# Kernel optimization log

Hardware: AMD Instinct MI355X
Metric: run time of the kernel (lower is better)

The kernel has to match this reference:

```python
import jax, jax.numpy as jnp
import numpy as np

SEQ_LEN = 96
D_MODEL = 512
BATCH = 512
FREQ = SEQ_LEN // 2 + 1  # 49
EPS = 1e-5


def setup_inputs() -> dict:
    key = jax.random.key(0)
    ks = jax.random.split(key, 9)
    s = 1.0 / np.sqrt(D_MODEL)
    return {
        "x": jax.random.normal(ks[0], (BATCH, SEQ_LEN, D_MODEL), jnp.float32),
        "freq_weights": jnp.ones((FREQ,), jnp.float32),
        "Wl": jax.random.normal(ks[1], (D_MODEL, D_MODEL), jnp.float32) * s,
        "bl": jax.random.normal(ks[2], (D_MODEL,), jnp.float32) * s,
        "Wh": jax.random.normal(ks[3], (D_MODEL, D_MODEL), jnp.float32) * s,
        "bh": jax.random.normal(ks[4], (D_MODEL,), jnp.float32) * s,
        "Wg": jax.random.normal(ks[5], (2 * D_MODEL, D_MODEL), jnp.float32) * s,
        "bg": jax.random.normal(ks[6], (D_MODEL,), jnp.float32) * s,
        "gamma": jnp.ones((D_MODEL,), jnp.float32),
        "beta": jnp.zeros((D_MODEL,), jnp.float32),
    }


def reference(x, freq_weights, Wl, bl, Wh, bh, Wg, bg, gamma, beta):
    # Batched rfft over seq axis for all channels at once: [B, F, D] complex
    xf = jnp.fft.rfft(x, axis=1)
    xw = xf * freq_weights[None, :, None]
    cutoff = FREQ // 3  # 16 (static)
    idx = jnp.arange(FREQ)[None, :, None]
    x_low_f = jnp.where(idx < cutoff, xw, 0)
    x_high_f = jnp.where(idx >= cutoff, xw, 0)
    x_low = jnp.fft.irfft(x_low_f, n=SEQ_LEN, axis=1)   # [B, S, D]
    x_high = jnp.fft.irfft(x_high_f, n=SEQ_LEN, axis=1)
    x_low = jnp.einsum("bsd,de->bse", x_low, Wl) + bl
    x_high = jnp.einsum("bsd,de->bse", x_high, Wh) + bh
    gate_in = jnp.concatenate([x_low, x_high], axis=-1)  # [B, S, 2D]
    gate = jax.nn.sigmoid(jnp.einsum("bsd,de->bse", gate_in, Wg) + bg)
    out = gate * x_low + (1.0 - gate) * x_high
    y = x + out  # dropout is identity in eval mode
    mu = jnp.mean(y, axis=-1, keepdims=True)
    var = jnp.var(y, axis=-1, keepdims=True)
    return (y - mu) / jnp.sqrt(var + EPS) * gamma + beta
```

## Files before the change

### kernel.cpp

```cpp
#include <hip/hip_runtime.h>

typedef unsigned short u16;
typedef unsigned int u32;

#define SEQ 96
#define DM 512
#define NBATCH 512
#define NFREQ 49
#define CUT 16
#define MROWS (NBATCH * SEQ)

typedef __attribute__((ext_vector_type(8))) short bf16x8;
typedef __attribute__((ext_vector_type(4))) float f32x4;

__device__ __forceinline__ u16 f2bf(float f) {
  u32 u = __float_as_uint(f);
  u32 r = (u + 0x7fffu + ((u >> 16) & 1u)) >> 16;
  return (u16)r;
}
__device__ __forceinline__ float bf2f(u16 u) {
  return __uint_as_float(((u32)u) << 16);
}

__device__ __forceinline__ void g2l16(const void* g, void* l) {
  __builtin_amdgcn_global_load_lds(
      (const __attribute__((address_space(1))) void*)g,
      (__attribute__((address_space(3))) void*)l, 16, 0, 0);
}

__global__ void build_filters_k(const float* __restrict__ w,
                                u16* __restrict__ FlB, u16* __restrict__ FhB) {
  int idx = blockIdx.x * 256 + threadIdx.x;
  if (idx >= SEQ * SEQ) return;
  int s = idx / SEQ, t = idx % SEQ;
  int d = s - t;
  const float scale = 1.0f / (float)SEQ;
  const float w0 = 6.283185307179586f / (float)SEQ;
  float cl = 0.f, ch = 0.f;
  for (int k = 0; k < NFREQ; k++) {
    int m = (k * d) % SEQ;
    if (m < 0) m += SEQ;
    float c = (k == 0 || k == SEQ / 2) ? 1.0f : 2.0f;
    float v = c * w[k] * cosf(w0 * (float)m) * scale;
    if (k < CUT) cl += v; else ch += v;
  }
  FlB[idx] = f2bf(cl);
  FhB[idx] = f2bf(ch);
}

__global__ void __launch_bounds__(256) transpose_w_k(
    const float* __restrict__ W, u16* __restrict__ Wt, int K, int N) {
  __shared__ float t[32][33];
  int k0 = blockIdx.x * 32, n0 = blockIdx.y * 32;
  int tx = threadIdx.x & 31, ty = threadIdx.x >> 5;
  #pragma unroll
  for (int r = 0; r < 32; r += 8)
    t[ty + r][tx] = W[(size_t)(k0 + ty + r) * N + n0 + tx];
  __syncthreads();
  #pragma unroll
  for (int r = 0; r < 32; r += 8)
    Wt[(size_t)(n0 + ty + r) * K + k0 + tx] = f2bf(t[tx][ty + r]);
}

__global__ void __launch_bounds__(256) xb_k(const float* __restrict__ x,
                                            u16* __restrict__ xb) {
  size_t t = ((size_t)blockIdx.x * 256 + threadIdx.x) * 8;
  float4 f0 = *(const float4*)(x + t);
  float4 f1 = *(const float4*)(x + t + 4);
  uint4 o;
  o.x = (u32)f2bf(f0.x) | ((u32)f2bf(f0.y) << 16);
  o.y = (u32)f2bf(f0.z) | ((u32)f2bf(f0.w) << 16);
  o.z = (u32)f2bf(f1.x) | ((u32)f2bf(f1.y) << 16);
  o.w = (u32)f2bf(f1.z) | ((u32)f2bf(f1.w) << 16);
  *(uint4*)(xb + t) = o;
}

__global__ void __launch_bounds__(256) proj_dual_k(
    const u16* __restrict__ xb, const u16* __restrict__ Wt,
    u16* __restrict__ uT, u16* __restrict__ vT) {
  __shared__ __align__(16) u16 As[128 * 64];
  __shared__ __align__(16) u16 Bs[128 * 64];
  const int m0 = blockIdx.x * 128;
  const int n0 = blockIdx.y * 128;
  const int tid = threadIdx.x;
  const int lane = tid & 63;
  const int w = tid >> 6;
  const int wm = w & 1, wn = w >> 1;
  const int l15 = lane & 15;
  const int lq = lane >> 4;

  f32x4 acc[4][4] = {};

  for (int kt = 0; kt < 512; kt += 64) {
    #pragma unroll
    for (int r = 0; r < 4; r++) {
      int c = r * 256 + tid;
      int row = c >> 3;
      int off = (c & 7) << 3;
      u32 lo = (u32)((r * 256 + w * 64) << 4);
      g2l16(xb + (size_t)(m0 + row) * 512 + kt + off, (char*)As + lo);
      g2l16(Wt + (size_t)(n0 + row) * 512 + kt + off, (char*)Bs + lo);
    }
    __syncthreads();
    #pragma unroll
    for (int kk = 0; kk < 64; kk += 32) {
      bf16x8 af[4], bf[4];
      #pragma unroll
      for (int i = 0; i < 4; i++)
        af[i] = *(const bf16x8*)&As[(wm * 64 + i * 16 + l15) * 64 + kk + lq * 8];
      #pragma unroll
      for (int j = 0; j < 4; j++)
        bf[j] = *(const bf16x8*)&Bs[(wn * 64 + j * 16 + l15) * 64 + kk + lq * 8];
      #pragma unroll
      for (int i = 0; i < 4; i++)
        #pragma unroll
        for (int j = 0; j < 4; j++)
          acc[i][j] = __builtin_amdgcn_mfma_f32_16x16x32_bf16(af[i], bf[j], acc[i][j], 0, 0, 0);
    }
    __syncthreads();
  }

  #pragma unroll
  for (int j = 0; j < 4; j++) {
    int nv = n0 + wn * 64 + j * 16 + l15;
    u16* dst = (nv < 512) ? uT : vT;
    int e = nv & 511;
    #pragma unroll
    for (int i = 0; i < 4; i++) {
      int mbase = m0 + wm * 64 + i * 16 + lq * 4;
      int b = mbase / 96, s = mbase % 96;
      ushort4 st;
      st.x = f2bf(acc[i][j][0]);
      st.y = f2bf(acc[i][j][1]);
      st.z = f2bf(acc[i][j][2]);
      st.w = f2bf(acc[i][j][3]);
      *(ushort4*)&dst[((size_t)b * 512 + e) * SEQ + s] = st;
    }
  }
}

__global__ void __launch_bounds__(256) filter2_k(
    const u16* __restrict__ uT, const u16* __restrict__ vT,
    const u16* __restrict__ FlB, const u16* __restrict__ FhB,
    const float* __restrict__ bl, const float* __restrict__ bh,
    u16* __restrict__ yl, u16* __restrict__ yh) {
  __shared__ __align__(16) u16 lds[2 * SEQ * SEQ + 2 * 64 * SEQ];
  u16* Fls = lds;
  u16* Bu = lds + 2 * SEQ * SEQ;
  u16* Bv = Bu + 64 * SEQ;
  const int tid = threadIdx.x;
  const int lane = tid & 63, w = tid >> 6;
  const int b = blockIdx.x, d0 = blockIdx.y * 64;

  #pragma unroll
  for (int it = 0; it < 9; it++) {
    int c = it * 256 + tid;
    const u16* src = (c < 1152) ? (FlB + c * 8) : (FhB + (c - 1152) * 8);
    g2l16(src, (char*)Fls + ((it * 256 + w * 64) << 4));
  }
  const u16* bu = uT + ((size_t)b * 512 + d0) * SEQ;
  const u16* bv = vT + ((size_t)b * 512 + d0) * SEQ;
  #pragma unroll
  for (int it = 0; it < 3; it++) {
    int c = it * 256 + tid;
    int row = c / 12, off = (c % 12) * 8;
    u32 lo = (u32)((it * 256 + w * 64) << 4);
    g2l16(bu + (size_t)row * SEQ + off, (char*)Bu + lo);
    g2l16(bv + (size_t)row * SEQ + off, (char*)Bv + lo);
  }
  __syncthreads();

  const int wf = w >> 1, wd = w & 1;
  const int l15 = lane & 15, lq = lane >> 4;
  const u16* F = wf ? (Fls + SEQ * SEQ) : Fls;
  const u16* Bsrc = wf ? Bv : Bu;
  f32x4 acc[6][2] = {};
  #pragma unroll
  for (int ks = 0; ks < 3; ks++) {
    int kt = ks * 32;
    bf16x8 bf[2];
    #pragma unroll
    for (int j = 0; j < 2; j++)
      bf[j] = *(const bf16x8*)&Bsrc[(wd * 32 + j * 16 + l15) * SEQ + kt + lq * 8];
    #pragma unroll
    for (int i = 0; i < 6; i++) {
      bf16x8 af = *(const bf16x8*)&F[(i * 16 + l15) * SEQ + kt + lq * 8];
      #pragma unroll
      for (int j = 0; j < 2; j++)
        acc[i][j] = __builtin_amdgcn_mfma_f32_16x16x32_bf16(af, bf[j], acc[i][j], 0, 0, 0);
    }
  }
  const float* bias = wf ? bh : bl;
  u16* dst = wf ? yh : yl;
  #pragma unroll
  for (int j = 0; j < 2; j++) {
    int d = d0 + wd * 32 + j * 16 + l15;
    float bv2 = bias[d];
    #pragma unroll
    for (int i = 0; i < 6; i++)
      #pragma unroll
      for (int r = 0; r < 4; r++) {
        int s = i * 16 + lq * 4 + r;
        dst[((size_t)b * SEQ + s) * DM + d] = f2bf(acc[i][j][r] + bv2);
      }
  }
}

__global__ void __launch_bounds__(256) gemm_gate_mfma_k(
    const u16* __restrict__ yl, const u16* __restrict__ yh,
    const u16* __restrict__ Wgt, const float* __restrict__ bg,
    u16* __restrict__ g) {
  __shared__ __align__(16) u16 As[128 * 64];
  __shared__ __align__(16) u16 Bs[128 * 64];
  const int m0 = blockIdx.x * 128;
  const int n0 = blockIdx.y * 128;
  const int tid = threadIdx.x;
  const int lane = tid & 63;
  const int w = tid >> 6;
  const int wm = w & 1, wn = w >> 1;
  const int l15 = lane & 15;
  const int lq = lane >> 4;

  f32x4 acc[4][4] = {};

  for (int kt = 0; kt < 1024; kt += 64) {
    const u16* Ak = (kt < 512) ? yl : yh;
    int ka = kt & 511;
    #pragma unroll
    for (int r = 0; r < 4; r++) {
      int c = r * 256 + tid;
      int row = c >> 3;
      int off = (c & 7) << 3;
      u32 lo = (u32)((r * 256 + w * 64) << 4);
      g2l16(Ak + (size_t)(m0 + row) * 512 + ka + off, (char*)As + lo);
      g2l16(Wgt + (size_t)(n0 + row) * 1024 + kt + off, (char*)Bs + lo);
    }
    __syncthreads();
    #pragma unroll
    for (int kk = 0; kk < 64; kk += 32) {
      bf16x8 af[4], bf[4];
      #pragma unroll
      for (int i = 0; i < 4; i++)
        af[i] = *(const bf16x8*)&As[(wm * 64 + i * 16 + l15) * 64 + kk + lq * 8];
      #pragma unroll
      for (int j = 0; j < 4; j++)
        bf[j] = *(const bf16x8*)&Bs[(wn * 64 + j * 16 + l15) * 64 + kk + lq * 8];
      #pragma unroll
      for (int i = 0; i < 4; i++)
        #pragma unroll
        for (int j = 0; j < 4; j++)
          acc[i][j] = __builtin_amdgcn_mfma_f32_16x16x32_bf16(af[i], bf[j], acc[i][j], 0, 0, 0);
    }
    __syncthreads();
  }

  #pragma unroll
  for (int j = 0; j < 4; j++) {
    int n = n0 + wn * 64 + j * 16 + l15;
    float bv = bg[n];
    #pragma unroll
    for (int i = 0; i < 4; i++) {
      int mrow = m0 + wm * 64 + i * 16 + lq * 4;
      #pragma unroll
      for (int r = 0; r < 4; r++) {
        float z = acc[i][j][r] + bv;
        g[(size_t)(mrow + r) * 512 + n] = f2bf(1.0f / (1.0f + __expf(-z)));
      }
    }
  }
}

__global__ void __launch_bounds__(256) final_ln_k(
    const float* __restrict__ x, const u16* __restrict__ yl,
    const u16* __restrict__ yh, const u16* __restrict__ g,
    const float* __restrict__ gamma, const float* __restrict__ beta,
    float* __restrict__ out) {
  __shared__ float red[8];
  int r = blockIdx.x;
  size_t base = (size_t)r * 512;
  float vv[2];
  float sum = 0.f, sumsq = 0.f;
  #pragma unroll
  for (int j = 0; j < 2; j++) {
    int e = threadIdx.x + j * 256;
    float lv = bf2f(yl[base + e]);
    float hv = bf2f(yh[base + e]);
    float gv = bf2f(g[base + e]);
    float v = x[base + e] + gv * lv + (1.f - gv) * hv;
    vv[j] = v;
    sum += v;
    sumsq += v * v;
  }
  #pragma unroll
  for (int off = 32; off; off >>= 1) {
    sum += __shfl_down(sum, off);
    sumsq += __shfl_down(sumsq, off);
  }
  int wid = threadIdx.x >> 6;
  if ((threadIdx.x & 63) == 0) {
    red[wid] = sum;
    red[4 + wid] = sumsq;
  }
  __syncthreads();
  sum = red[0] + red[1] + red[2] + red[3];
  sumsq = red[4] + red[5] + red[6] + red[7];
  float mu = sum * (1.f / 512.f);
  float var = sumsq * (1.f / 512.f) - mu * mu;
  float inv = rsqrtf(var + 1e-5f);
  #pragma unroll
  for (int j = 0; j < 2; j++) {
    int e = threadIdx.x + j * 256;
    out[base + e] = (vv[j] - mu) * inv * gamma[e] + beta[e];
  }
}

extern "C" void kernel_launch(void* const* d_in, const int* in_sizes, int n_in,
                              void* d_out, int out_size, void* d_ws, size_t ws_size,
                              hipStream_t stream) {
  const float* x     = (const float*)d_in[0];
  const float* fw    = (const float*)d_in[1];
  const float* Wl    = (const float*)d_in[2];
  const float* bl    = (const float*)d_in[3];
  const float* Wh    = (const float*)d_in[4];
  const float* bh    = (const float*)d_in[5];
  const float* Wg    = (const float*)d_in[6];
  const float* bg    = (const float*)d_in[7];
  const float* gamma = (const float*)d_in[8];
  const float* beta  = (const float*)d_in[9];
  float* out = (float*)d_out;

  char* ws = (char*)d_ws;
  u16* FlB = (u16*)ws;
  u16* FhB = FlB + SEQ * SEQ;
  u16* Wt  = (u16*)(ws + 64 * 1024);
  u16* Wgt = Wt + 1024 * 512;
  size_t tsz = (size_t)MROWS * 512;
  u16* xb = (u16*)(ws + 4 * 1024 * 1024);
  u16* uT = xb + tsz;
  u16* vT = uT + tsz;
  u16* yh = vT + tsz;
  u16* yl = xb;
  u16* gb = uT;

  build_filters_k<<<dim3(36), dim3(256), 0, stream>>>(fw, FlB, FhB);
  transpose_w_k<<<dim3(16, 16), dim3(256), 0, stream>>>(Wl, Wt, 512, 512);
  transpose_w_k<<<dim3(16, 16), dim3(256), 0, stream>>>(Wh, Wt + 512 * 512, 512, 512);
  transpose_w_k<<<dim3(32, 16), dim3(256), 0, stream>>>(Wg, Wgt, 1024, 512);
  xb_k<<<dim3(MROWS * 512 / 2048), dim3(256), 0, stream>>>(x, xb);
  proj_dual_k<<<dim3(MROWS / 128, 8), dim3(256), 0, stream>>>(xb, Wt, uT, vT);
  filter2_k<<<dim3(NBATCH, DM / 64), dim3(256), 0, stream>>>(
      uT, vT, FlB, FhB, bl, bh, yl, yh);
  gemm_gate_mfma_k<<<dim3(MROWS / 128, 4), dim3(256), 0, stream>>>(yl, yh, Wgt, bg, gb);
  final_ln_k<<<dim3(MROWS), dim3(256), 0, stream>>>(x, yl, yh, gb, gamma, beta, out);
}
```

Baseline: 494.3 us.

## Fold gate GEMM into projection via precomputed Wl·Wg, Wh·Wg and fused tail

Uses linearity to precompute Wl@Wg_top and Wh@Wg_bot plus a combined gate bias, so the gate pre-activation becomes the filtered projections of x through these product matrices. A single wide GEMM now converts x to bf16 on the fly and produces four projections (u, v, p1, p2). One tail kernel per batch applies the low/high filters with MFMA, then computes the gate, the mix and the residual into the output. LayerNorm runs in place afterward. This drops the separate bf16 conversion, the 1024-K gate GEMM and the bf16 intermediates, at the cost of a wider projection GEMM (N=2048) and more bf16 rounding through the product weights.

```diff
diff --git a/kernel.cpp b/kernel.cpp
--- a/kernel.cpp
+++ b/kernel.cpp
@@ -17,9 +17,6 @@
   u32 u = __float_as_uint(f);
   u32 r = (u + 0x7fffu + ((u >> 16) & 1u)) >> 16;
   return (u16)r;
-}
-__device__ __forceinline__ float bf2f(u16 u) {
-  return __uint_as_float(((u32)u) << 16);
 }
 
 __device__ __forceinline__ void g2l16(const void* g, void* l) {
@@ -48,6 +45,60 @@
   FhB[idx] = f2bf(ch);
 }
 
+__global__ void __launch_bounds__(256) smallgemm_k(
+    const float* __restrict__ Wl, const float* __restrict__ Wh,
+    const float* __restrict__ Wg, float* __restrict__ A1f,
+    float* __restrict__ A2f) {
+  const float* A = blockIdx.z ? Wh : Wl;
+  const float* B = Wg + (size_t)blockIdx.z * 512 * 512;
+  float* O = blockIdx.z ? A2f : A1f;
+  __shared__ float As[64][16];
+  __shared__ float Bs[16][64];
+  int i0 = blockIdx.x * 64, j0 = blockIdx.y * 64;
+  int tid = threadIdx.x;
+  int tx = tid & 15, ty = tid >> 4;
+  float acc[4][4] = {};
+  for (int k0 = 0; k0 < 512; k0 += 16) {
+    __syncthreads();
+    #pragma unroll
+    for (int v = 0; v < 4; v++) {
+      int c = v * 256 + tid;
+      As[c >> 4][c & 15] = A[(size_t)(i0 + (c >> 4)) * 512 + k0 + (c & 15)];
+      Bs[c >> 6][c & 63] = B[(size_t)(k0 + (c >> 6)) * 512 + j0 + (c & 63)];
+    }
+    __syncthreads();
+    #pragma unroll
+    for (int kk = 0; kk < 16; kk++) {
+      float av[4], bv[4];
+      #pragma unroll
+      for (int ii = 0; ii < 4; ii++) av[ii] = As[ty * 4 + ii][kk];
+      #pragma unroll
+      for (int jj = 0; jj < 4; jj++) bv[jj] = Bs[kk][tx * 4 + jj];
+      #pragma unroll
+      for (int ii = 0; ii < 4; ii++)
+        #pragma unroll
+        for (int jj = 0; jj < 4; jj++)
+          acc[ii][jj] = fmaf(av[ii], bv[jj], acc[ii][jj]);
+    }
+  }
+  #pragma unroll
+  for (int ii = 0; ii < 4; ii++)
+    #pragma unroll
+    for (int jj = 0; jj < 4; jj++)
+      O[(size_t)(i0 + ty * 4 + ii) * 512 + j0 + tx * 4 + jj] = acc[ii][jj];
+}
+
+__global__ void __launch_bounds__(256) cbias_k(
+    const float* __restrict__ bl, const float* __restrict__ bh,
+    const float* __restrict__ Wg, const float* __restrict__ bg,
+    float* __restrict__ cb) {
+  int j = blockIdx.x * 256 + threadIdx.x;
+  float acc = bg[j];
+  for (int k = 0; k < 512; k++) acc = fmaf(bl[k], Wg[(size_t)k * 512 + j], acc);
+  for (int k = 0; k < 512; k++) acc = fmaf(bh[k], Wg[(size_t)(512 + k) * 512 + j], acc);
+  cb[j] = acc;
+}
+
 __global__ void __launch_bounds__(256) transpose_w_k(
     const float* __restrict__ W, u16* __restrict__ Wt, int K, int N) {
   __shared__ float t[32][33];
@@ -62,26 +113,14 @@
     Wt[(size_t)(n0 + ty + r) * K + k0 + tx] = f2bf(t[tx][ty + r]);
 }
 
-__global__ void __launch_bounds__(256) xb_k(const float* __restrict__ x,
-                                            u16* __restrict__ xb) {
-  size_t t = ((size_t)blockIdx.x * 256 + threadIdx.x) * 8;
-  float4 f0 = *(const float4*)(x + t);
-  float4 f1 = *(const float4*)(x + t + 4);
-  uint4 o;
-  o.x = (u32)f2bf(f0.x) | ((u32)f2bf(f0.y) << 16);
-  o.y = (u32)f2bf(f0.z) | ((u32)f2bf(f0.w) << 16);
-  o.z = (u32)f2bf(f1.x) | ((u32)f2bf(f1.y) << 16);
-  o.w = (u32)f2bf(f1.z) | ((u32)f2bf(f1.w) << 16);
-  *(uint4*)(xb + t) = o;
-}
-
-__global__ void __launch_bounds__(256) proj_dual_k(
-    const u16* __restrict__ xb, const u16* __restrict__ Wt,
-    u16* __restrict__ uT, u16* __restrict__ vT) {
-  __shared__ __align__(16) u16 As[128 * 64];
-  __shared__ __align__(16) u16 Bs[128 * 64];
-  const int m0 = blockIdx.x * 128;
-  const int n0 = blockIdx.y * 128;
+__global__ void __launch_bounds__(256, 2) mega_k(
+    const float* __restrict__ x, const u16* __restrict__ W4t,
+    u16* __restrict__ uT, u16* __restrict__ vT,
+    u16* __restrict__ p1T, u16* __restrict__ p2T) {
+  __shared__ __align__(16) u16 As[256 * 32];
+  __shared__ __align__(16) u16 Bs[128 * 32];
+  const int n0 = blockIdx.x * 128;
+  const int m0 = blockIdx.y * 256;
   const int tid = threadIdx.x;
   const int lane = tid & 63;
   const int w = tid >> 6;
@@ -89,46 +128,55 @@
   const int l15 = lane & 15;
   const int lq = lane >> 4;
 
-  f32x4 acc[4][4] = {};
-
-  for (int kt = 0; kt < 512; kt += 64) {
-    #pragma unroll
-    for (int r = 0; r < 4; r++) {
+  f32x4 acc[8][4] = {};
+
+  for (int kt = 0; kt < 512; kt += 32) {
+    #pragma unroll
+    for (int it = 0; it < 4; it++) {
+      int u = it * 256 + tid;
+      int row = u >> 2, k8 = (u & 3) << 3;
+      const float* src = x + (size_t)(m0 + row) * 512 + kt + k8;
+      float4 f0 = *(const float4*)src;
+      float4 f1 = *(const float4*)(src + 4);
+      uint4 o;
+      o.x = (u32)f2bf(f0.x) | ((u32)f2bf(f0.y) << 16);
+      o.y = (u32)f2bf(f0.z) | ((u32)f2bf(f0.w) << 16);
+      o.z = (u32)f2bf(f1.x) | ((u32)f2bf(f1.y) << 16);
+      o.w = (u32)f2bf(f1.z) | ((u32)f2bf(f1.w) << 16);
+      *(uint4*)&As[row * 32 + k8] = o;
+    }
+    #pragma unroll
+    for (int r = 0; r < 2; r++) {
       int c = r * 256 + tid;
-      int row = c >> 3;
-      int off = (c & 7) << 3;
+      int row = c >> 2, off = (c & 3) << 3;
       u32 lo = (u32)((r * 256 + w * 64) << 4);
-      g2l16(xb + (size_t)(m0 + row) * 512 + kt + off, (char*)As + lo);
-      g2l16(Wt + (size_t)(n0 + row) * 512 + kt + off, (char*)Bs + lo);
+      g2l16(W4t + (size_t)(n0 + row) * 512 + kt + off, (char*)Bs + lo);
     }
     __syncthreads();
-    #pragma unroll
-    for (int kk = 0; kk < 64; kk += 32) {
-      bf16x8 af[4], bf[4];
-      #pragma unroll
-      for (int i = 0; i < 4; i++)
-        af[i] = *(const bf16x8*)&As[(wm * 64 + i * 16 + l15) * 64 + kk + lq * 8];
+    bf16x8 af[8], bf[4];
+    #pragma unroll
+    for (int i = 0; i < 8; i++)
+      af[i] = *(const bf16x8*)&As[(wm * 128 + i * 16 + l15) * 32 + lq * 8];
+    #pragma unroll
+    for (int j = 0; j < 4; j++)
+      bf[j] = *(const bf16x8*)&Bs[(wn * 64 + j * 16 + l15) * 32 + lq * 8];
+    #pragma unroll
+    for (int i = 0; i < 8; i++)
       #pragma unroll
       for (int j = 0; j < 4; j++)
-        bf[j] = *(const bf16x8*)&Bs[(wn * 64 + j * 16 + l15) * 64 + kk + lq * 8];
-      #pragma unroll
-      for (int i = 0; i < 4; i++)
-        #pragma unroll
-        for (int j = 0; j < 4; j++)
-          acc[i][j] = __builtin_amdgcn_mfma_f32_16x16x32_bf16(af[i], bf[j], acc[i][j], 0, 0, 0);
-    }
+        acc[i][j] = __builtin_amdgcn_mfma_f32_16x16x32_bf16(af[i], bf[j], acc[i][j], 0, 0, 0);
     __syncthreads();
   }
 
+  u16* dst = (n0 < 512) ? uT : (n0 < 1024) ? vT : (n0 < 1536) ? p1T : p2T;
+  const int e0 = (n0 & 511) + wn * 64;
   #pragma unroll
   for (int j = 0; j < 4; j++) {
-    int nv = n0 + wn * 64 + j * 16 + l15;
-    u16* dst = (nv < 512) ? uT : vT;
-    int e = nv & 511;
-    #pragma unroll
-    for (int i = 0; i < 4; i++) {
-      int mbase = m0 + wm * 64 + i * 16 + lq * 4;
-      int b = mbase / 96, s = mbase % 96;
+    int e = e0 + j * 16 + l15;
+    #pragma unroll
+    for (int i = 0; i < 8; i++) {
+      int m = m0 + wm * 128 + i * 16 + lq * 4;
+      int b = m / 96, s = m - b * 96;
       ushort4 st;
       st.x = f2bf(acc[i][j][0]);
       st.y = f2bf(acc[i][j][1]);
@@ -139,154 +187,78 @@
   }
 }
 
-__global__ void __launch_bounds__(256) filter2_k(
+__global__ void __launch_bounds__(256) tail_k(
     const u16* __restrict__ uT, const u16* __restrict__ vT,
-    const u16* __restrict__ FlB, const u16* __restrict__ FhB,
-    const float* __restrict__ bl, const float* __restrict__ bh,
-    u16* __restrict__ yl, u16* __restrict__ yh) {
-  __shared__ __align__(16) u16 lds[2 * SEQ * SEQ + 2 * 64 * SEQ];
-  u16* Fls = lds;
-  u16* Bu = lds + 2 * SEQ * SEQ;
-  u16* Bv = Bu + 64 * SEQ;
+    const u16* __restrict__ p1T, const u16* __restrict__ p2T,
+    const u16* __restrict__ FlB, const float* __restrict__ bl,
+    const float* __restrict__ bh, const float* __restrict__ cb,
+    const float* __restrict__ x, float* __restrict__ y) {
+  __shared__ __align__(16) u16 F[2 * SEQ * SEQ];
   const int tid = threadIdx.x;
   const int lane = tid & 63, w = tid >> 6;
-  const int b = blockIdx.x, d0 = blockIdx.y * 64;
+  const int l15 = lane & 15, lq = lane >> 4;
+  const int b = blockIdx.x;
 
   #pragma unroll
   for (int it = 0; it < 9; it++) {
     int c = it * 256 + tid;
-    const u16* src = (c < 1152) ? (FlB + c * 8) : (FhB + (c - 1152) * 8);
-    g2l16(src, (char*)Fls + ((it * 256 + w * 64) << 4));
-  }
-  const u16* bu = uT + ((size_t)b * 512 + d0) * SEQ;
-  const u16* bv = vT + ((size_t)b * 512 + d0) * SEQ;
-  #pragma unroll
-  for (int it = 0; it < 3; it++) {
-    int c = it * 256 + tid;
-    int row = c / 12, off = (c % 12) * 8;
-    u32 lo = (u32)((it * 256 + w * 64) << 4);
-    g2l16(bu + (size_t)row * SEQ + off, (char*)Bu + lo);
-    g2l16(bv + (size_t)row * SEQ + off, (char*)Bv + lo);
+    g2l16(FlB + c * 8, (char*)F + ((it * 256 + w * 64) << 4));
   }
   __syncthreads();
 
-  const int wf = w >> 1, wd = w & 1;
-  const int l15 = lane & 15, lq = lane >> 4;
-  const u16* F = wf ? (Fls + SEQ * SEQ) : Fls;
-  const u16* Bsrc = wf ? Bv : Bu;
-  f32x4 acc[6][2] = {};
-  #pragma unroll
-  for (int ks = 0; ks < 3; ks++) {
-    int kt = ks * 32;
-    bf16x8 bf[2];
-    #pragma unroll
-    for (int j = 0; j < 2; j++)
-      bf[j] = *(const bf16x8*)&Bsrc[(wd * 32 + j * 16 + l15) * SEQ + kt + lq * 8];
-    #pragma unroll
-    for (int i = 0; i < 6; i++) {
-      bf16x8 af = *(const bf16x8*)&F[(i * 16 + l15) * SEQ + kt + lq * 8];
-      #pragma unroll
-      for (int j = 0; j < 2; j++)
-        acc[i][j] = __builtin_amdgcn_mfma_f32_16x16x32_bf16(af, bf[j], acc[i][j], 0, 0, 0);
-    }
-  }
-  const float* bias = wf ? bh : bl;
-  u16* dst = wf ? yh : yl;
-  #pragma unroll
-  for (int j = 0; j < 2; j++) {
-    int d = d0 + wd * 32 + j * 16 + l15;
-    float bv2 = bias[d];
+  for (int ch = 0; ch < 8; ch++) {
+    int d0c = ch * 64 + w * 16;
+    const u16* bu = uT + ((size_t)b * 512 + d0c) * SEQ;
+    const u16* bv = vT + ((size_t)b * 512 + d0c) * SEQ;
+    const u16* bp1 = p1T + ((size_t)b * 512 + d0c) * SEQ;
+    const u16* bp2 = p2T + ((size_t)b * 512 + d0c) * SEQ;
+    f32x4 accl[6] = {}, acch[6] = {}, accg[6] = {};
+    #pragma unroll
+    for (int ks = 0; ks < 3; ks++) {
+      int kt = ks * 32;
+      int boff = l15 * SEQ + kt + lq * 8;
+      bf16x8 BU = *(const bf16x8*)&bu[boff];
+      bf16x8 BV = *(const bf16x8*)&bv[boff];
+      bf16x8 BP1 = *(const bf16x8*)&bp1[boff];
+      bf16x8 BP2 = *(const bf16x8*)&bp2[boff];
+      #pragma unroll
+      for (int i = 0; i < 6; i++) {
+        int aoff = (i * 16 + l15) * SEQ + kt + lq * 8;
+        bf16x8 afl = *(const bf16x8*)&F[aoff];
+        bf16x8 afh = *(const bf16x8*)&F[SEQ * SEQ + aoff];
+        accl[i] = __builtin_amdgcn_mfma_f32_16x16x32_bf16(afl, BU, accl[i], 0, 0, 0);
+        acch[i] = __builtin_amdgcn_mfma_f32_16x16x32_bf16(afh, BV, acch[i], 0, 0, 0);
+        accg[i] = __builtin_amdgcn_mfma_f32_16x16x32_bf16(afl, BP1, accg[i], 0, 0, 0);
+        accg[i] = __builtin_amdgcn_mfma_f32_16x16x32_bf16(afh, BP2, accg[i], 0, 0, 0);
+      }
+    }
+    int d = d0c + l15;
+    float blv = bl[d], bhv = bh[d], cbv = cb[d];
     #pragma unroll
     for (int i = 0; i < 6; i++)
       #pragma unroll
       for (int r = 0; r < 4; r++) {
         int s = i * 16 + lq * 4 + r;
-        dst[((size_t)b * SEQ + s) * DM + d] = f2bf(acc[i][j][r] + bv2);
+        size_t idx = ((size_t)b * SEQ + s) * 512 + d;
+        float ylv = accl[i][r] + blv;
+        float yhv = acch[i][r] + bhv;
+        float gv = 1.0f / (1.0f + __expf(-(accg[i][r] + cbv)));
+        y[idx] = x[idx] + gv * ylv + (1.0f - gv) * yhv;
       }
   }
 }
 
-__global__ void __launch_bounds__(256) gemm_gate_mfma_k(
-    const u16* __restrict__ yl, const u16* __restrict__ yh,
-    const u16* __restrict__ Wgt, const float* __restrict__ bg,
-    u16* __restrict__ g) {
-  __shared__ __align__(16) u16 As[128 * 64];
-  __shared__ __align__(16) u16 Bs[128 * 64];
-  const int m0 = blockIdx.x * 128;
-  const int n0 = blockIdx.y * 128;
-  const int tid = threadIdx.x;
-  const int lane = tid & 63;
-  const int w = tid >> 6;
-  const int wm = w & 1, wn = w >> 1;
-  const int l15 = lane & 15;
-  const int lq = lane >> 4;
-
-  f32x4 acc[4][4] = {};
-
-  for (int kt = 0; kt < 1024; kt += 64) {
-    const u16* Ak = (kt < 512) ? yl : yh;
-    int ka = kt & 511;
-    #pragma unroll
-    for (int r = 0; r < 4; r++) {
-      int c = r * 256 + tid;
-      int row = c >> 3;
-      int off = (c & 7) << 3;
-      u32 lo = (u32)((r * 256 + w * 64) << 4);
-      g2l16(Ak + (size_t)(m0 + row) * 512 + ka + off, (char*)As + lo);
-      g2l16(Wgt + (size_t)(n0 + row) * 1024 + kt + off, (char*)Bs + lo);
-    }
-    __syncthreads();
-    #pragma unroll
-    for (int kk = 0; kk < 64; kk += 32) {
-      bf16x8 af[4], bf[4];
-      #pragma unroll
-      for (int i = 0; i < 4; i++)
-        af[i] = *(const bf16x8*)&As[(wm * 64 + i * 16 + l15) * 64 + kk + lq * 8];
-      #pragma unroll
-      for (int j = 0; j < 4; j++)
-        bf[j] = *(const bf16x8*)&Bs[(wn * 64 + j * 16 + l15) * 64 + kk + lq * 8];
-      #pragma unroll
-      for (int i = 0; i < 4; i++)
-        #pragma unroll
-        for (int j = 0; j < 4; j++)
-          acc[i][j] = __builtin_amdgcn_mfma_f32_16x16x32_bf16(af[i], bf[j], acc[i][j], 0, 0, 0);
-    }
-    __syncthreads();
-  }
-
-  #pragma unroll
-  for (int j = 0; j < 4; j++) {
-    int n = n0 + wn * 64 + j * 16 + l15;
-    float bv = bg[n];
-    #pragma unroll
-    for (int i = 0; i < 4; i++) {
-      int mrow = m0 + wm * 64 + i * 16 + lq * 4;
-      #pragma unroll
-      for (int r = 0; r < 4; r++) {
-        float z = acc[i][j][r] + bv;
-        g[(size_t)(mrow + r) * 512 + n] = f2bf(1.0f / (1.0f + __expf(-z)));
-      }
-    }
-  }
-}
-
-__global__ void __launch_bounds__(256) final_ln_k(
-    const float* __restrict__ x, const u16* __restrict__ yl,
-    const u16* __restrict__ yh, const u16* __restrict__ g,
-    const float* __restrict__ gamma, const float* __restrict__ beta,
-    float* __restrict__ out) {
+__global__ void __launch_bounds__(256) ln_inplace_k(
+    float* __restrict__ y, const float* __restrict__ gamma,
+    const float* __restrict__ beta) {
   __shared__ float red[8];
-  int r = blockIdx.x;
-  size_t base = (size_t)r * 512;
+  size_t base = (size_t)blockIdx.x * 512;
   float vv[2];
   float sum = 0.f, sumsq = 0.f;
   #pragma unroll
   for (int j = 0; j < 2; j++) {
     int e = threadIdx.x + j * 256;
-    float lv = bf2f(yl[base + e]);
-    float hv = bf2f(yh[base + e]);
-    float gv = bf2f(g[base + e]);
-    float v = x[base + e] + gv * lv + (1.f - gv) * hv;
+    float v = y[base + e];
     vv[j] = v;
     sum += v;
     sumsq += v * v;
@@ -310,7 +282,7 @@
   #pragma unroll
   for (int j = 0; j < 2; j++) {
     int e = threadIdx.x + j * 256;
-    out[base + e] = (vv[j] - mu) * inv * gamma[e] + beta[e];
+    y[base + e] = (vv[j] - mu) * inv * gamma[e] + beta[e];
   }
 }
 
@@ -332,24 +304,24 @@
   char* ws = (char*)d_ws;
   u16* FlB = (u16*)ws;
   u16* FhB = FlB + SEQ * SEQ;
-  u16* Wt  = (u16*)(ws + 64 * 1024);
-  u16* Wgt = Wt + 1024 * 512;
+  float* cb  = (float*)(ws + 40960);
+  float* A1f = (float*)(ws + 1 * 1024 * 1024);
+  float* A2f = (float*)(ws + 2 * 1024 * 1024);
+  u16* W4t = (u16*)(ws + 4 * 1024 * 1024);
   size_t tsz = (size_t)MROWS * 512;
-  u16* xb = (u16*)(ws + 4 * 1024 * 1024);
-  u16* uT = xb + tsz;
-  u16* vT = uT + tsz;
-  u16* yh = vT + tsz;
-  u16* yl = xb;
-  u16* gb = uT;
+  u16* uT  = (u16*)(ws + 8 * 1024 * 1024);
+  u16* vT  = uT + tsz;
+  u16* p1T = vT + tsz;
+  u16* p2T = p1T + tsz;
 
   build_filters_k<<<dim3(36), dim3(256), 0, stream>>>(fw, FlB, FhB);
-  transpose_w_k<<<dim3(16, 16), dim3(256), 0, stream>>>(Wl, Wt, 512, 512);
-  transpose_w_k<<<dim3(16, 16), dim3(256), 0, stream>>>(Wh, Wt + 512 * 512, 512, 512);
-  transpose_w_k<<<dim3(32, 16), dim3(256), 0, stream>>>(Wg, Wgt, 1024, 512);
-  xb_k<<<dim3(MROWS * 512 / 2048), dim3(256), 0, stream>>>(x, xb);
-  proj_dual_k<<<dim3(MROWS / 128, 8), dim3(256), 0, stream>>>(xb, Wt, uT, vT);
-  filter2_k<<<dim3(NBATCH, DM / 64), dim3(256), 0, stream>>>(
-      uT, vT, FlB, FhB, bl, bh, yl, yh);
-  gemm_gate_mfma_k<<<dim3(MROWS / 128, 4), dim3(256), 0, stream>>>(yl, yh, Wgt, bg, gb);
-  final_ln_k<<<dim3(MROWS), dim3(256), 0, stream>>>(x, yl, yh, gb, gamma, beta, out);
-}
+  smallgemm_k<<<dim3(8, 8, 2), dim3(256), 0, stream>>>(Wl, Wh, Wg, A1f, A2f);
+  cbias_k<<<dim3(2), dim3(256), 0, stream>>>(bl, bh, Wg, bg, cb);
+  transpose_w_k<<<dim3(16, 16), dim3(256), 0, stream>>>(Wl, W4t, 512, 512);
+  transpose_w_k<<<dim3(16, 16), dim3(256), 0, stream>>>(Wh, W4t + 512 * 512, 512, 512);
+  transpose_w_k<<<dim3(16, 16), dim3(256), 0, stream>>>(A1f, W4t + 2 * 512 * 512, 512, 512);
+  transpose_w_k<<<dim3(16, 16), dim3(256), 0, stream>>>(A2f, W4t + 3 * 512 * 512, 512, 512);
+  mega_k<<<dim3(16, MROWS / 256), dim3(256), 0, stream>>>(x, W4t, uT, vT, p1T, p2T);
+  tail_k<<<dim3(NBATCH), dim3(256), 0, stream>>>(uT, vT, p1T, p2T, FlB, bl, bh, cb, x, out);
+  ln_inplace_k<<<dim3(MROWS), dim3(256), 0, stream>>>(out, gamma, beta);
+}
```

Result: slower. 635.5 us (+28.6%).
